# Performance work log

Hardware: AMD Instinct MI355X
Metric: run time of the kernel (lower is better)

The kernel has to match this reference:

```python
import jax, jax.numpy as jnp
import numpy as np

SELF_OBS_DIM = 18
NEIGHBOR_OBS_DIM = 6
HIDDEN = 256
NUM_NEIGHBORS = 6
BATCH = 131072


def setup_inputs() -> dict:
    key = jax.random.key(0)
    k1, k2, k3, k4, k5, k6 = jax.random.split(key, 6)
    obs_dim = SELF_OBS_DIM + NEIGHBOR_OBS_DIM * NUM_NEIGHBORS
    self_obs = jax.random.normal(k1, (BATCH, SELF_OBS_DIM), dtype=jnp.float32)
    obs = jax.random.normal(k2, (BATCH, obs_dim), dtype=jnp.float32)
    # MLP params (PyTorch Linear default init scale ~ 1/sqrt(fan_in))
    W1 = jax.random.uniform(k3, (NEIGHBOR_OBS_DIM, HIDDEN), minval=-1.0, maxval=1.0) / np.sqrt(NEIGHBOR_OBS_DIM)
    b1 = jax.random.uniform(k4, (HIDDEN,), minval=-1.0, maxval=1.0) / np.sqrt(NEIGHBOR_OBS_DIM)
    W2 = jax.random.uniform(k5, (HIDDEN, HIDDEN), minval=-1.0, maxval=1.0) / np.sqrt(HIDDEN)
    b2 = jax.random.uniform(k6, (HIDDEN,), minval=-1.0, maxval=1.0) / np.sqrt(HIDDEN)
    return {
        "self_obs": self_obs,
        "obs": obs,
        "W1": W1.astype(jnp.float32),
        "b1": b1.astype(jnp.float32),
        "W2": W2.astype(jnp.float32),
        "b2": b2.astype(jnp.float32),
        "all_neighbor_obs_size": NEIGHBOR_OBS_DIM * NUM_NEIGHBORS,
        "batch_size": BATCH,
    }


def reference(self_obs, obs, W1, b1, W2, b2, all_neighbor_obs_size, batch_size):
    # slice out neighbor observations: obs[:, self_obs_dim : self_obs_dim + all_neighbor_obs_size]
    obs_neighbors = obs[:, SELF_OBS_DIM:SELF_OBS_DIM + all_neighbor_obs_size]
    # reshape to per-neighbor rows: [B * num_neighbors, neighbor_obs_dim]
    x = obs_neighbors.reshape(-1, NEIGHBOR_OBS_DIM)
    # shared 2-layer MLP with tanh (sample-factory default nonlinearity)
    h = jnp.tanh(x @ W1 + b1)
    h = jnp.tanh(h @ W2 + b2)
    # [B, num_neighbors, hidden] -> mean over neighbor axis
    neighbor_embeds = h.reshape(batch_size, -1, HIDDEN)
    mean_embed = jnp.mean(neighbor_embeds, axis=1)
    return mean_embed
```

## Files before the change

### kernel.cpp

```cpp
#include <hip/hip_runtime.h>


#define HID     256
#define OBSD    54
#define SELFD   18
#define TILE_B  8
#define TILE_R  48
#define LDA     264
#define BATCHN  131072
#define NTILES  (BATCHN / TILE_B)
#define GRID_WG 2048
#define TANH_K  2.8853900817779268f

typedef __attribute__((ext_vector_type(8))) short bf16x8;
typedef __attribute__((ext_vector_type(4))) float f32x4;

__device__ __forceinline__ unsigned cvt_pk_bf16(float lo, float hi) {
    unsigned r;
    asm("v_cvt_pk_bf16_f32 %0, %1, %2" : "=v"(r) : "v"(lo), "v"(hi));
    return r;
}

__device__ __forceinline__ float tanh_fused(float x, float bK) {
    float t = __builtin_amdgcn_exp2f(__builtin_fmaf(x, TANH_K, bK));
    return 1.0f - 2.0f * __builtin_amdgcn_rcpf(t + 1.0f);
}

__device__ __forceinline__ unsigned bfbits(float f) {
    unsigned u = __float_as_uint(f);
    u += 0x7fffu + ((u >> 16) & 1u);
    return u >> 16;
}

__global__ void prep(const float* __restrict__ W1, const float* __restrict__ W2,
                     short* __restrict__ w1t, short* __restrict__ w2t) {
    int idx = blockIdx.x * 256 + threadIdx.x;
    if (idx < 65536) {
        int n = idx >> 8, k = idx & 255;
        w2t[idx] = (short)bfbits(W2[k * HID + n]);
    } else {
        int j = idx - 65536;
        int n = j >> 5, k = j & 31;
        w1t[j] = (k < 6) ? (short)bfbits(W1[k * HID + n]) : (short)0;
    }
}

__global__ __launch_bounds__(512, 4) void qenc_main(
        const float* __restrict__ obs,
        const short* __restrict__ w1t,
        const float* __restrict__ b1,
        const short* __restrict__ w2t,
        const float* __restrict__ b2,
        float* __restrict__ out)
{
    __shared__ short a[TILE_R * LDA];

    const int tid  = threadIdx.x;
    const int wave = tid >> 6;
    const int lane = tid & 63;
    const int q    = lane >> 4;
    const int c16  = lane & 15;
    const int colbase = wave * 32;

    bf16x8 Bf[8][2];
    #pragma unroll
    for (int kk = 0; kk < 8; ++kk)
        #pragma unroll
        for (int ct = 0; ct < 2; ++ct)
            Bf[kk][ct] = *(const bf16x8*)
                (w2t + (colbase + ct * 16 + c16) * HID + kk * 32 + q * 8);

    bf16x8 B1f[2];
    #pragma unroll
    for (int ct = 0; ct < 2; ++ct)
        B1f[ct] = *(const bf16x8*)(w1t + (colbase + ct * 16 + c16) * 32 + q * 8);

    float b1s[2][4];
    #pragma unroll
    for (int ct = 0; ct < 2; ++ct)
        #pragma unroll
        for (int g = 0; g < 4; ++g)
            b1s[ct][g] = b1[colbase + ct * 16 + q * 4 + g] * TANH_K;
    float b2s[2];
    #pragma unroll
    for (int ct = 0; ct < 2; ++ct)
        b2s[ct] = b2[colbase + ct * 16 + c16] * TANH_K;

    int soff[3];
    #pragma unroll
    for (int rt = 0; rt < 3; ++rt) {
        int row = rt * 16 + c16;
        soff[rt] = (row / 6) * OBSD + SELFD + (row % 6) * 6;
    }

    const int blA = 2 * q + (q & 1);
    const int blB = (q < 2) ? (q + 5) : (q - 1);
    const bool isq0 = (q == 0), isq1 = (q == 1), isq2 = (q == 2);

    for (int tile = blockIdx.x; tile < NTILES; tile += GRID_WG) {
        const size_t obase = (size_t)tile * (TILE_B * OBSD);

        #pragma unroll
        for (int rt = 0; rt < 3; ++rt) {
            const float* src = obs + obase + soff[rt];
            float2 f0 = *(const float2*)(src);
            float2 f1 = *(const float2*)(src + 2);
            float2 f2 = *(const float2*)(src + 4);
            union { unsigned w[4]; bf16x8 v; } xf;
            xf.w[0] = cvt_pk_bf16(f0.x, f0.y);
            xf.w[1] = cvt_pk_bf16(f1.x, f1.y);
            xf.w[2] = cvt_pk_bf16(f2.x, f2.y);
            xf.w[3] = 0u;
            #pragma unroll
            for (int ct = 0; ct < 2; ++ct) {
                f32x4 c = __builtin_amdgcn_mfma_f32_16x16x32_bf16(
                    B1f[ct], xf.v, (f32x4){0.f, 0.f, 0.f, 0.f}, 0, 0, 0);
                float t0 = tanh_fused(c[0], b1s[ct][0]);
                float t1 = tanh_fused(c[1], b1s[ct][1]);
                float t2 = tanh_fused(c[2], b1s[ct][2]);
                float t3 = tanh_fused(c[3], b1s[ct][3]);
                uint2 dd;
                dd.x = cvt_pk_bf16(t0, t1);
                dd.y = cvt_pk_bf16(t2, t3);
                *(uint2*)&a[(rt * 16 + c16) * LDA + colbase + ct * 16 + q * 4] = dd;
            }
        }
        __syncthreads();

        f32x4 acc[3][2];
        #pragma unroll
        for (int rt = 0; rt < 3; ++rt)
            #pragma unroll
            for (int ct = 0; ct < 2; ++ct) acc[rt][ct] = (f32x4){0.f, 0.f, 0.f, 0.f};

        #pragma unroll
        for (int kk = 0; kk < 8; ++kk) {
            bf16x8 Af[3];
            #pragma unroll
            for (int rt = 0; rt < 3; ++rt)
                Af[rt] = *(const bf16x8*)&a[(rt * 16 + c16) * LDA + kk * 32 + q * 8];
            #pragma unroll
            for (int rt = 0; rt < 3; ++rt)
                #pragma unroll
                for (int ct = 0; ct < 2; ++ct)
                    acc[rt][ct] = __builtin_amdgcn_mfma_f32_16x16x32_bf16(
                        Af[rt], Bf[kk][ct], acc[rt][ct], 0, 0, 0);
        }

        const int b0 = tile * TILE_B;
        #pragma unroll
        for (int ct = 0; ct < 2; ++ct) {
            const int col = colbase + ct * 16 + c16;
            float s[3], uu[3], f[3];
            #pragma unroll
            for (int rt = 0; rt < 3; ++rt) {
                float t0 = tanh_fused(acc[rt][ct][0], b2s[ct]);
                float t1 = tanh_fused(acc[rt][ct][1], b2s[ct]);
                float t2 = tanh_fused(acc[rt][ct][2], b2s[ct]);
                float t3 = tanh_fused(acc[rt][ct][3], b2s[ct]);
                s[rt] = t0 + t1; uu[rt] = t2 + t3; f[rt] = s[rt] + uu[rt];
            }
            float A = isq1 ? s[0] : f[0];
            float B = isq1 ? uu[0] : (isq2 ? f[1] : s[1]);
            float C = isq2 ? s[2] : (isq1 ? f[1] : uu[1]);
            float D = isq2 ? uu[2] : f[2];
            float p1 = isq0 ? C : (isq1 ? A : (isq2 ? D : B));
            float p2 = (q < 2) ? B : C;
            float r1 = __shfl_xor(p1, 16);
            float r2 = __shfl_xor(p2, 48);
            float own1 = (isq0 ? A : (isq1 ? C : (isq2 ? B : D))) + r1;
            float own2 = ((q < 2) ? D : A) + r2;
            out[(size_t)(b0 + blA) * HID + col] = own1 * (1.0f / 6.0f);
            out[(size_t)(b0 + blB) * HID + col] = own2 * (1.0f / 6.0f);
        }
        __syncthreads();
    }
}

extern "C" void kernel_launch(void* const* d_in, const int* in_sizes, int n_in,
                              void* d_out, int out_size, void* d_ws, size_t ws_size,
                              hipStream_t stream) {
    const float* obs = (const float*)d_in[1];
    const float* W1  = (const float*)d_in[2];
    const float* b1  = (const float*)d_in[3];
    const float* W2  = (const float*)d_in[4];
    const float* b2  = (const float*)d_in[5];
    float* outp = (float*)d_out;

    short* w2t = (short*)d_ws;
    short* w1t = (short*)((char*)d_ws + 131072);

    prep<<<288, 256, 0, stream>>>(W1, W2, w1t, w2t);
    qenc_main<<<GRID_WG, 512, 0, stream>>>(obs, w1t, b1, w2t, b2, outp);
}
```

Measured before the change: 335.1 us.

## Fold tanh scale into weights, bias into MFMA accumulator, double-buffer LDS

Pre-scales W1 and W2 by the tanh exponent constant in the prep kernel and seeds the MFMA accumulators with the scaled biases. This removes the per-element FMA before each exp2. It also ping-pongs between two LDS buffers so the trailing __syncthreads per tile can be dropped. The cost is double the LDS footprint, which may reduce occupancy at 4 blocks per CU. Rounding W to bf16 after scaling also slightly changes numerics.

```diff
diff --git a/kernel.cpp b/kernel.cpp
--- a/kernel.cpp
+++ b/kernel.cpp
@@ -21,8 +21,8 @@
     return r;
 }
 
-__device__ __forceinline__ float tanh_fused(float x, float bK) {
-    float t = __builtin_amdgcn_exp2f(__builtin_fmaf(x, TANH_K, bK));
+__device__ __forceinline__ float tanh_z(float z) {
+    float t = __builtin_amdgcn_exp2f(z);
     return 1.0f - 2.0f * __builtin_amdgcn_rcpf(t + 1.0f);
 }
 
@@ -37,11 +37,11 @@
     int idx = blockIdx.x * 256 + threadIdx.x;
     if (idx < 65536) {
         int n = idx >> 8, k = idx & 255;
-        w2t[idx] = (short)bfbits(W2[k * HID + n]);
+        w2t[idx] = (short)bfbits(W2[k * HID + n] * TANH_K);
     } else {
         int j = idx - 65536;
         int n = j >> 5, k = j & 31;
-        w1t[j] = (k < 6) ? (short)bfbits(W1[k * HID + n]) : (short)0;
+        w1t[j] = (k < 6) ? (short)bfbits(W1[k * HID + n] * TANH_K) : (short)0;
     }
 }
 
@@ -53,7 +53,7 @@
         const float* __restrict__ b2,
         float* __restrict__ out)
 {
-    __shared__ short a[TILE_R * LDA];
+    __shared__ short a2[2][TILE_R * LDA];
 
     const int tid  = threadIdx.x;
     const int wave = tid >> 6;
@@ -97,8 +97,10 @@
     const int blB = (q < 2) ? (q + 5) : (q - 1);
     const bool isq0 = (q == 0), isq1 = (q == 1), isq2 = (q == 2);
 
+    int pb = 0;
     for (int tile = blockIdx.x; tile < NTILES; tile += GRID_WG) {
         const size_t obase = (size_t)tile * (TILE_B * OBSD);
+        short* __restrict__ a = a2[pb];
 
         #pragma unroll
         for (int rt = 0; rt < 3; ++rt) {
@@ -114,11 +116,13 @@
             #pragma unroll
             for (int ct = 0; ct < 2; ++ct) {
                 f32x4 c = __builtin_amdgcn_mfma_f32_16x16x32_bf16(
-                    B1f[ct], xf.v, (f32x4){0.f, 0.f, 0.f, 0.f}, 0, 0, 0);
-                float t0 = tanh_fused(c[0], b1s[ct][0]);
-                float t1 = tanh_fused(c[1], b1s[ct][1]);
-                float t2 = tanh_fused(c[2], b1s[ct][2]);
-                float t3 = tanh_fused(c[3], b1s[ct][3]);
+                    B1f[ct], xf.v,
+                    (f32x4){b1s[ct][0], b1s[ct][1], b1s[ct][2], b1s[ct][3]},
+                    0, 0, 0);
+                float t0 = tanh_z(c[0]);
+                float t1 = tanh_z(c[1]);
+                float t2 = tanh_z(c[2]);
+                float t3 = tanh_z(c[3]);
                 uint2 dd;
                 dd.x = cvt_pk_bf16(t0, t1);
                 dd.y = cvt_pk_bf16(t2, t3);
@@ -131,7 +135,8 @@
         #pragma unroll
         for (int rt = 0; rt < 3; ++rt)
             #pragma unroll
-            for (int ct = 0; ct < 2; ++ct) acc[rt][ct] = (f32x4){0.f, 0.f, 0.f, 0.f};
+            for (int ct = 0; ct < 2; ++ct)
+                acc[rt][ct] = (f32x4){b2s[ct], b2s[ct], b2s[ct], b2s[ct]};
 
         #pragma unroll
         for (int kk = 0; kk < 8; ++kk) {
@@ -154,10 +159,10 @@
             float s[3], uu[3], f[3];
             #pragma unroll
             for (int rt = 0; rt < 3; ++rt) {
-                float t0 = tanh_fused(acc[rt][ct][0], b2s[ct]);
-                float t1 = tanh_fused(acc[rt][ct][1], b2s[ct]);
-                float t2 = tanh_fused(acc[rt][ct][2], b2s[ct]);
-                float t3 = tanh_fused(acc[rt][ct][3], b2s[ct]);
+                float t0 = tanh_z(acc[rt][ct][0]);
+                float t1 = tanh_z(acc[rt][ct][1]);
+                float t2 = tanh_z(acc[rt][ct][2]);
+                float t3 = tanh_z(acc[rt][ct][3]);
                 s[rt] = t0 + t1; uu[rt] = t2 + t3; f[rt] = s[rt] + uu[rt];
             }
             float A = isq1 ? s[0] : f[0];
@@ -173,7 +178,7 @@
             out[(size_t)(b0 + blA) * HID + col] = own1 * (1.0f / 6.0f);
             out[(size_t)(b0 + blB) * HID + col] = own2 * (1.0f / 6.0f);
         }
-        __syncthreads();
+        pb ^= 1;
     }
 }
 
```

New measurement: 341.6 us. About the same (+2.0%).
